# Kernel tuning notes

Measured on AMD Instinct MI355X. Metric: run time of the kernel, lower is better.

The kernel has to match this reference:

```python
import math
import jax, jax.numpy as jnp
import numpy as np

N_HEADS = 16
N_KV_HEADS = 4
HEAD_DIM = 64
DIM = 1024
WINDOW = 16
EPS = 0.01


def _alibi_slopes(n_heads):
    closest = 2 ** math.floor(math.log2(n_heads))
    base = 2.0 ** (-2.0 ** (-(math.log2(closest) - 3)))
    slopes = base ** np.arange(1, closest + 1, dtype=np.float32)
    if closest < n_heads:
        eb = 2.0 ** (-2.0 ** (-(math.log2(2 * closest) - 3)))
        extra = eb ** np.arange(1, 2 * (n_heads - closest) + 1, 2, dtype=np.float32)
        slopes = np.concatenate([slopes, extra])
    return jnp.asarray(slopes[:n_heads])


def _rmsnorm(x, w):
    xf = x.astype(jnp.float32)
    norm = jax.lax.rsqrt(jnp.mean(xf * xf, axis=-1, keepdims=True) + EPS)
    return (xf * norm).astype(x.dtype) * w


def setup_inputs() -> dict:
    key = jax.random.key(0)
    ks = jax.random.split(key, 6)
    B, L = 2, 2048
    s = 1.0 / math.sqrt(DIM)
    return {
        "x": jax.random.normal(ks[0], (B, L, DIM), jnp.float32),
        "wq": jax.random.normal(ks[1], (N_HEADS * HEAD_DIM, DIM), jnp.float32) * s,
        "wk": jax.random.normal(ks[2], (N_KV_HEADS * HEAD_DIM, DIM), jnp.float32) * s,
        "wv": jax.random.normal(ks[3], (N_KV_HEADS * HEAD_DIM, DIM), jnp.float32) * s,
        "wo": jax.random.normal(ks[4], (DIM, N_HEADS * HEAD_DIM), jnp.float32) * s,
        "q_norm_w": jnp.ones((HEAD_DIM,), jnp.float32),
        "k_norm_w": jnp.ones((HEAD_DIM,), jnp.float32),
    }


def reference(x, wq, wk, wv, wo, q_norm_w, k_norm_w):
    B, L, _ = x.shape
    n_rep = N_HEADS // N_KV_HEADS
    q = (x @ wq.T).reshape(B, L, N_HEADS, HEAD_DIM)
    k = (x @ wk.T).reshape(B, L, N_KV_HEADS, HEAD_DIM)
    v = (x @ wv.T).reshape(B, L, N_KV_HEADS, HEAD_DIM)
    q = _rmsnorm(q, q_norm_w)
    k = _rmsnorm(k, k_norm_w)
    # GQA repeat: head h maps to kv head (h % n_kv_heads), matching torch expand order
    k = jnp.broadcast_to(k[:, :, None], (B, L, n_rep, N_KV_HEADS, HEAD_DIM)).reshape(B, L, N_HEADS, HEAD_DIM)
    v = jnp.broadcast_to(v[:, :, None], (B, L, n_rep, N_KV_HEADS, HEAD_DIM)).reshape(B, L, N_HEADS, HEAD_DIM)
    # ALiBi bias with causal + sliding-window mask
    pos = jnp.arange(L)
    rel = pos[None, :] - pos[:, None]  # [L, L], j - i
    slopes = _alibi_slopes(N_HEADS)  # [H]
    bias = slopes[:, None, None] * rel[None].astype(jnp.float32)  # [H, L, L]
    masked = (rel > 0) | (rel < -WINDOW)
    bias = jnp.where(masked[None], -jnp.inf, bias)
    scale = 1.0 / math.sqrt(HEAD_DIM)
    attn = jnp.einsum("bqhd,bkhd->bhqk", q, k) * scale + bias[None]
    attn = jax.nn.softmax(attn, axis=-1)
    out = jnp.einsum("bhqk,bkhd->bqhd", attn, v).reshape(B, L, N_HEADS * HEAD_DIM)
    return out @ wo.T
```

## Files before the change

kernel.cpp:

```cpp
#include <hip/hip_runtime.h>
#include <math.h>

#define DIM 1024
#define NH 16
#define NKV 4
#define HD 64
#define WINDOW 16
#define EPS 0.01f

typedef __bf16 bf16_t;
typedef bf16_t bf16x8 __attribute__((ext_vector_type(8)));
typedef bf16_t bf16x4 __attribute__((ext_vector_type(4)));
typedef float f32x4 __attribute__((ext_vector_type(4)));

__global__ __launch_bounds__(256) void f2bf_all(const float* __restrict__ x,
                                                const float* __restrict__ wq,
                                                const float* __restrict__ wk,
                                                const float* __restrict__ wv,
                                                const float* __restrict__ wo,
                                                bf16_t* __restrict__ xb,
                                                bf16_t* __restrict__ wqkvb,
                                                bf16_t* __restrict__ wob) {
  int i = blockIdx.x * blockDim.x + threadIdx.x;
  const float* src;
  bf16_t* dst;
  int off;
  if (i < 1048576) { src = x; dst = xb; off = i; }
  else if (i < 1310720) { src = wq; dst = wqkvb; off = i - 1048576; }
  else if (i < 1376256) { src = wk; dst = wqkvb + (size_t)1024 * DIM; off = i - 1310720; }
  else if (i < 1441792) { src = wv; dst = wqkvb + (size_t)1280 * DIM; off = i - 1376256; }
  else { src = wo; dst = wob; off = i - 1441792; }
  float4 f = ((const float4*)src)[off];
  bf16x4 o = {(bf16_t)f.x, (bf16_t)f.y, (bf16_t)f.z, (bf16_t)f.w};
  ((bf16x4*)dst)[off] = o;
}


#define GEMM_STAGE(buf, Ag, Bg)                                                 \
  {                                                                             \
    _Pragma("unroll")                                                           \
    for (int it = 0; it < 4; it++) {                                            \
      int c = it * 256 + t;                                                     \
      int r = c >> 3;                                                           \
      int kc = ((c & 7) - r) & 7;                                               \
      __builtin_amdgcn_global_load_lds(                                         \
          (const __attribute__((address_space(1))) void*)((Ag) + (size_t)r * K + kc * 8), \
          (__attribute__((address_space(3))) void*)(As[buf] + c * 8), 16, 0, 0); \
    }                                                                           \
    _Pragma("unroll")                                                           \
    for (int it = 0; it < 2; it++) {                                            \
      int c = it * 256 + t;                                                     \
      int r = c >> 3;                                                           \
      int kc = ((c & 7) - r) & 7;                                               \
      __builtin_amdgcn_global_load_lds(                                         \
          (const __attribute__((address_space(1))) void*)((Bg) + (size_t)r * K + kc * 8), \
          (__attribute__((address_space(3))) void*)(Bs[buf] + c * 8), 16, 0, 0); \
    }                                                                           \
  }

#define GEMM_DBUF_LOOP(Aptr, Bptr)                                              \
  {                                                                             \
    const bf16_t* Abase = Aptr + (size_t)row0 * K;                              \
    const bf16_t* Bbase = Bptr + (size_t)col0 * K;                              \
    GEMM_STAGE(0, Abase, Bbase)                                                 \
    const int nIter = K >> 6;                                                   \
    for (int ki = 0; ki < nIter; ki++) {                                        \
      __syncthreads();                                                          \
      if (ki + 1 < nIter)                                                       \
        GEMM_STAGE((ki + 1) & 1, Abase + (ki + 1) * 64, Bbase + (ki + 1) * 64)  \
      const bf16_t* Ab = As[ki & 1];                                            \
      const bf16_t* Bb = Bs[ki & 1];                                            \
      _Pragma("unroll")                                                         \
      for (int h = 0; h < 2; h++) {                                             \
        bf16x8 af[2], bfr[4];                                                   \
        _Pragma("unroll")                                                       \
        for (int mi = 0; mi < 2; mi++) af[mi] = *(const bf16x8*)(Ab + aoff[h][mi]); \
        _Pragma("unroll")                                                       \
        for (int ni = 0; ni < 4; ni++) bfr[ni] = *(const bf16x8*)(Bb + boff[h][ni]); \
        _Pragma("unroll")                                                       \
        for (int mi = 0; mi < 2; mi++)                                          \
          _Pragma("unroll")                                                     \
          for (int ni = 0; ni < 4; ni++)                                        \
            acc[mi][ni] = __builtin_amdgcn_mfma_f32_16x16x32_bf16(af[mi], bfr[ni], \
                                                                  acc[mi][ni], 0, 0, 0); \
      }                                                                         \
    }                                                                           \
  }

#define GEMM_PROLOGUE(NBX, BYX)                                                 \
  const int t = threadIdx.x;                                                    \
  const int lane = t & 63;                                                      \
  const int wid = t >> 6;                                                       \
  const int xcd = blockIdx.x & 7;                                               \
  const int jj = blockIdx.x >> 3;                                               \
  const int bx = jj % (NBX);                                                    \
  const int row0 = (xcd * (BYX) + jj / (NBX)) * 128;                            \
  const int col0 = bx * 64;                                                     \
  const int wm = wid * 32;                                                      \
  const int lquad = lane >> 4;                                                  \
  const int lcol = lane & 15;                                                   \
  int aoff[2][2], boff[2][4];                                                   \
  _Pragma("unroll")                                                             \
  for (int h = 0; h < 2; h++) {                                                 \
    _Pragma("unroll")                                                           \
    for (int mi = 0; mi < 2; mi++) {                                            \
      int r = wm + mi * 16 + lcol;                                              \
      aoff[h][mi] = r * 64 + (((h * 4 + lquad) + r) & 7) * 8;                   \
    }                                                                           \
    _Pragma("unroll")                                                           \
    for (int ni = 0; ni < 4; ni++) {                                            \
      int r = ni * 16 + lcol;                                                   \
      boff[h][ni] = r * 64 + (((h * 4 + lquad) + r) & 7) * 8;                   \
    }                                                                           \
  }                                                                             \
  f32x4 acc[2][4] = {};

__global__ __launch_bounds__(256) void gemm_qkv_rms(const bf16_t* __restrict__ A,
                                                    const bf16_t* __restrict__ B,
                                                    bf16_t* __restrict__ C,
                                                    const float* __restrict__ qw,
                                                    const float* __restrict__ kw,
                                                    int M, int N, int K) {
  __shared__ bf16_t As[2][128 * 64];
  __shared__ bf16_t Bs[2][64 * 64];
  GEMM_PROLOGUE(24, 4)
  GEMM_DBUF_LOOP(A, B)

  const int hcol = bx;
  const bool isv = (hcol >= 20);
  float wreg[4];
  if (!isv) {
    const float* wp = (hcol < 16) ? qw : kw;
#pragma unroll
    for (int ni = 0; ni < 4; ni++) wreg[ni] = wp[ni * 16 + lcol];
  }

#pragma unroll
  for (int mi = 0; mi < 2; mi++) {
#pragma unroll
    for (int r = 0; r < 4; r++) {
      float norm = 1.0f;
      if (!isv) {
        float ss = 0.0f;
#pragma unroll
        for (int ni = 0; ni < 4; ni++) ss += acc[mi][ni][r] * acc[mi][ni][r];
#pragma unroll
        for (int off = 8; off >= 1; off >>= 1) ss += __shfl_xor(ss, off);
        norm = rsqrtf(ss * (1.0f / 64.0f) + EPS);
      }
      size_t base = (size_t)(row0 + wm + mi * 16 + lquad * 4 + r) * N + col0 + lcol;
#pragma unroll
      for (int ni = 0; ni < 4; ni++) {
        float v = acc[mi][ni][r] * norm;
        if (!isv) v *= wreg[ni];
        C[base + ni * 16] = (bf16_t)v;
      }
    }
  }
}

template <typename CT, int NBX, int BYX>
__global__ __launch_bounds__(256) void gemm_bf16(const bf16_t* __restrict__ A,
                                                 const bf16_t* __restrict__ B,
                                                 CT* __restrict__ C,
                                                 int M, int N, int K) {
  __shared__ bf16_t As[2][128 * 64];
  __shared__ bf16_t Bs[2][64 * 64];
  GEMM_PROLOGUE(NBX, BYX)
  GEMM_DBUF_LOOP(A, B)

#pragma unroll
  for (int mi = 0; mi < 2; mi++)
#pragma unroll
    for (int ni = 0; ni < 4; ni++) {
      size_t base = (size_t)(row0 + wm + mi * 16 + lquad * 4) * N + col0 + ni * 16 + lcol;
#pragma unroll
      for (int r = 0; r < 4; r++)
        C[base + (size_t)r * N] = (CT)acc[mi][ni][r];
    }
}

#define LKP 72
#define LVP 40

__global__ __launch_bounds__(1024) void attn_mfma(const bf16_t* __restrict__ qkv,
                                                  bf16_t* __restrict__ y) {
  __shared__ bf16_t Ks[4][32][LKP];
  __shared__ bf16_t VTs[4][64][LVP];
  __shared__ bf16_t Ps[16][16][LVP];

  const int t = threadIdx.x;
  const int lane = t & 63;
  const int w = t >> 6;
  const int b = blockIdx.x >> 7;
  const int i0loc = (blockIdx.x & 127) << 4;
  const int rowbase = b << 11;
  const int rowg0 = rowbase + i0loc;

  {
    int kvh = t >> 8;
    int key = (t >> 3) & 31;
    int dc = t & 7;
    int jloc = i0loc - 16 + key;
    int rg = rowbase + (jloc < 0 ? 0 : jloc);
    const bf16_t* src = qkv + (size_t)rg * 1536 + 1024 + kvh * 64 + dc * 8;
    bf16x8 kval = *(const bf16x8*)src;
    *(bf16x8*)(&Ks[kvh][key][dc * 8]) = kval;
    bf16x8 vval = *(const bf16x8*)(src + 256);
    int kslot = ((key >> 3) ^ (dc & 3)) * 8 + (key & 7);
#pragma unroll
    for (int e = 0; e < 8; e++) VTs[kvh][dc * 8 + e][kslot] = vval[e];
  }
  __syncthreads();

  const int col = lane & 15;
  const int quad = lane >> 4;
  const int h = w;
  const int kvh = w & 3;
  const float slope = exp2f(-0.5f * (float)(h + 1));

  bf16x8 kf[2][2];
#pragma unroll
  for (int kt = 0; kt < 2; kt++)
#pragma unroll
    for (int kc = 0; kc < 2; kc++)
      kf[kt][kc] = *(const bf16x8*)(&Ks[kvh][kt * 16 + col][kc * 32 + quad * 8]);
  bf16x8 vf[4];
#pragma unroll
  for (int nt = 0; nt < 4; nt++) {
    int dim = nt * 16 + col;
    int kchunk = quad ^ ((dim >> 3) & 3);
    vf[nt] = *(const bf16x8*)(&VTs[kvh][dim][kchunk * 8]);
  }

  const bf16_t* qrow = qkv + (size_t)(rowg0 + col) * 1536 + h * 64;
  bf16x8 qf0 = *(const bf16x8*)(qrow + quad * 8);
  bf16x8 qf1 = *(const bf16x8*)(qrow + 32 + quad * 8);

  f32x4 s0 = {}, s1 = {};
  s0 = __builtin_amdgcn_mfma_f32_16x16x32_bf16(qf0, kf[0][0], s0, 0, 0, 0);
  s0 = __builtin_amdgcn_mfma_f32_16x16x32_bf16(qf1, kf[0][1], s0, 0, 0, 0);
  s1 = __builtin_amdgcn_mfma_f32_16x16x32_bf16(qf0, kf[1][0], s1, 0, 0, 0);
  s1 = __builtin_amdgcn_mfma_f32_16x16x32_bf16(qf1, kf[1][1], s1, 0, 0, 0);

  const bool t0dead = (i0loc == 0);
  float sc0[4], sc1[4];
#pragma unroll
  for (int r = 0; r < 4; r++) {
    int rel0 = col - 16 - (quad * 4 + r);
    int rel1 = rel0 + 16;
    bool m0 = t0dead || (rel0 < -WINDOW);
    bool m1 = (rel1 > 0);
    sc0[r] = m0 ? -INFINITY : s0[r] * 0.125f + slope * (float)rel0;
    sc1[r] = m1 ? -INFINITY : s1[r] * 0.125f + slope * (float)rel1;
  }
  float mx[4], sum[4], p0[4], p1[4];
#pragma unroll
  for (int r = 0; r < 4; r++) mx[r] = fmaxf(sc0[r], sc1[r]);
#pragma unroll
  for (int off = 8; off >= 1; off >>= 1)
#pragma unroll
    for (int r = 0; r < 4; r++) mx[r] = fmaxf(mx[r], __shfl_xor(mx[r], off));
#pragma unroll
  for (int r = 0; r < 4; r++) {
    p0[r] = __expf(sc0[r] - mx[r]);
    p1[r] = __expf(sc1[r] - mx[r]);
    sum[r] = p0[r] + p1[r];
  }
#pragma unroll
  for (int off = 8; off >= 1; off >>= 1)
#pragma unroll
    for (int r = 0; r < 4; r++) sum[r] += __shfl_xor(sum[r], off);

#pragma unroll
  for (int r = 0; r < 4; r++) {
    Ps[w][quad * 4 + r][col] = (bf16_t)p0[r];
    Ps[w][quad * 4 + r][16 + col] = (bf16_t)p1[r];
  }
  bf16x8 pf = *(const bf16x8*)(&Ps[w][col][quad * 8]);

  f32x4 o[4] = {};
#pragma unroll
  for (int nt = 0; nt < 4; nt++)
    o[nt] = __builtin_amdgcn_mfma_f32_16x16x32_bf16(pf, vf[nt], o[nt], 0, 0, 0);

#pragma unroll
  for (int nt = 0; nt < 4; nt++)
#pragma unroll
    for (int r = 0; r < 4; r++)
      y[(size_t)(rowg0 + quad * 4 + r) * 1024 + h * 64 + nt * 16 + col] =
          (bf16_t)(o[nt][r] / sum[r]);
}

extern "C" void kernel_launch(void* const* d_in, const int* in_sizes, int n_in,
                              void* d_out, int out_size, void* d_ws, size_t ws_size,
                              hipStream_t stream) {
  const float* x  = (const float*)d_in[0];
  const float* wq = (const float*)d_in[1];
  const float* wk = (const float*)d_in[2];
  const float* wv = (const float*)d_in[3];
  const float* wo = (const float*)d_in[4];
  const float* qw = (const float*)d_in[5];
  const float* kw = (const float*)d_in[6];
  float* out = (float*)d_out;

  const int M = 4096;

  bf16_t* xb    = (bf16_t*)d_ws;
  bf16_t* wqkvb = xb + (size_t)M * DIM;
  bf16_t* wob   = wqkvb + (size_t)1536 * DIM;
  bf16_t* qkv   = wob + (size_t)DIM * DIM;
  bf16_t* yb    = qkv + (size_t)M * 1536;

  dim3 blk(256);
  f2bf_all<<<1703936 / 256, blk, 0, stream>>>(x, wq, wk, wv, wo, xb, wqkvb, wob);

  gemm_qkv_rms<<<768, blk, 0, stream>>>(xb, wqkvb, qkv, qw, kw, M, 1536, DIM);

  attn_mfma<<<256, dim3(1024), 0, stream>>>(qkv, yb);

  gemm_bf16<float, 16, 4><<<512, blk, 0, stream>>>(yb, wob, out, M, DIM, DIM);
}
```

Measured before the change: 126.8 us.

## Split GEMM K-halves across warp pairs with LDS reduction; hoist attention Q loads

Result: slower. 458.8 us (+261.7%).

```diff
diff --git a/kernel.cpp b/kernel.cpp
--- a/kernel.cpp
+++ b/kernel.cpp
@@ -70,21 +70,39 @@
         GEMM_STAGE((ki + 1) & 1, Abase + (ki + 1) * 64, Bbase + (ki + 1) * 64)  \
       const bf16_t* Ab = As[ki & 1];                                            \
       const bf16_t* Bb = Bs[ki & 1];                                            \
-      _Pragma("unroll")                                                         \
-      for (int h = 0; h < 2; h++) {                                             \
-        bf16x8 af[2], bfr[4];                                                   \
+      bf16x8 af[4], bfr[4];                                                     \
+      _Pragma("unroll")                                                         \
+      for (int mi = 0; mi < 4; mi++) af[mi] = *(const bf16x8*)(Ab + aoff[mi]);  \
+      _Pragma("unroll")                                                         \
+      for (int ni = 0; ni < 4; ni++) bfr[ni] = *(const bf16x8*)(Bb + boff[ni]); \
+      _Pragma("unroll")                                                         \
+      for (int mi = 0; mi < 4; mi++)                                            \
         _Pragma("unroll")                                                       \
-        for (int mi = 0; mi < 2; mi++) af[mi] = *(const bf16x8*)(Ab + aoff[h][mi]); \
-        _Pragma("unroll")                                                       \
-        for (int ni = 0; ni < 4; ni++) bfr[ni] = *(const bf16x8*)(Bb + boff[h][ni]); \
-        _Pragma("unroll")                                                       \
-        for (int mi = 0; mi < 2; mi++)                                          \
-          _Pragma("unroll")                                                     \
-          for (int ni = 0; ni < 4; ni++)                                        \
-            acc[mi][ni] = __builtin_amdgcn_mfma_f32_16x16x32_bf16(af[mi], bfr[ni], \
-                                                                  acc[mi][ni], 0, 0, 0); \
+        for (int ni = 0; ni < 4; ni++)                                          \
+          acc[mi][ni] = __builtin_amdgcn_mfma_f32_16x16x32_bf16(af[mi], bfr[ni], \
+                                                                acc[mi][ni], 0, 0, 0); \
+    }                                                                           \
+  }
+
+#define GEMM_REDUCE()                                                           \
+  {                                                                             \
+    float* Xs = (float*)smem;                                                   \
+    __syncthreads();                                                            \
+    _Pragma("unroll")                                                           \
+    for (int j = 0; j < 2; j++)                                                 \
+      _Pragma("unroll")                                                         \
+      for (int ni = 0; ni < 4; ni++)                                            \
+        *(f32x4*)(Xs + (size_t)(wid * 64 + ni * 16 + lcol) * 36 + j * 16 + lquad * 4) = \
+            acc[h0 ? j : 2 + j][ni];                                            \
+    __syncthreads();                                                            \
+    _Pragma("unroll")                                                           \
+    for (int j = 0; j < 2; j++)                                                 \
+      _Pragma("unroll")                                                         \
+      for (int ni = 0; ni < 4; ni++) {                                          \
+        f32x4 p = *(const f32x4*)(Xs + (size_t)((wid ^ 1) * 64 + ni * 16 + lcol) * 36 + \
+                                  j * 16 + lquad * 4);                          \
+        acc[j][ni] = (h0 ? acc[2 + j][ni] : acc[j][ni]) + p;                    \
       }                                                                         \
-    }                                                                           \
   }
 
 #define GEMM_PROLOGUE(NBX, BYX)                                                 \
@@ -96,35 +114,36 @@
   const int bx = jj % (NBX);                                                    \
   const int row0 = (xcd * (BYX) + jj / (NBX)) * 128;                            \
   const int col0 = bx * 64;                                                     \
+  const int pr = (wid >> 1) * 64;                                               \
+  const int h0 = wid & 1;                                                       \
   const int wm = wid * 32;                                                      \
   const int lquad = lane >> 4;                                                  \
   const int lcol = lane & 15;                                                   \
-  int aoff[2][2], boff[2][4];                                                   \
+  int aoff[4], boff[4];                                                         \
   _Pragma("unroll")                                                             \
-  for (int h = 0; h < 2; h++) {                                                 \
-    _Pragma("unroll")                                                           \
-    for (int mi = 0; mi < 2; mi++) {                                            \
-      int r = wm + mi * 16 + lcol;                                              \
-      aoff[h][mi] = r * 64 + (((h * 4 + lquad) + r) & 7) * 8;                   \
-    }                                                                           \
-    _Pragma("unroll")                                                           \
-    for (int ni = 0; ni < 4; ni++) {                                            \
-      int r = ni * 16 + lcol;                                                   \
-      boff[h][ni] = r * 64 + (((h * 4 + lquad) + r) & 7) * 8;                   \
-    }                                                                           \
+  for (int mi = 0; mi < 4; mi++) {                                              \
+    int r = pr + mi * 16 + lcol;                                                \
+    aoff[mi] = r * 64 + (((h0 * 4 + lquad) + r) & 7) * 8;                       \
   }                                                                             \
-  f32x4 acc[2][4] = {};
-
-__global__ __launch_bounds__(256) void gemm_qkv_rms(const bf16_t* __restrict__ A,
-                                                    const bf16_t* __restrict__ B,
-                                                    bf16_t* __restrict__ C,
-                                                    const float* __restrict__ qw,
-                                                    const float* __restrict__ kw,
-                                                    int M, int N, int K) {
-  __shared__ bf16_t As[2][128 * 64];
-  __shared__ bf16_t Bs[2][64 * 64];
+  _Pragma("unroll")                                                             \
+  for (int ni = 0; ni < 4; ni++) {                                              \
+    int r = ni * 16 + lcol;                                                     \
+    boff[ni] = r * 64 + (((h0 * 4 + lquad) + r) & 7) * 8;                       \
+  }                                                                             \
+  f32x4 acc[4][4] = {};
+
+__global__ __launch_bounds__(256, 3) void gemm_qkv_rms(const bf16_t* __restrict__ A,
+                                                       const bf16_t* __restrict__ B,
+                                                       bf16_t* __restrict__ C,
+                                                       const float* __restrict__ qw,
+                                                       const float* __restrict__ kw,
+                                                       int M, int N, int K) {
+  __shared__ __align__(16) char smem[49152];
+  bf16_t (*As)[128 * 64] = (bf16_t(*)[128 * 64])smem;
+  bf16_t (*Bs)[64 * 64] = (bf16_t(*)[64 * 64])(smem + 32768);
   GEMM_PROLOGUE(24, 4)
   GEMM_DBUF_LOOP(A, B)
+  GEMM_REDUCE()
 
   const int hcol = bx;
   const bool isv = (hcol >= 20);
@@ -160,14 +179,16 @@
 }
 
 template <typename CT, int NBX, int BYX>
-__global__ __launch_bounds__(256) void gemm_bf16(const bf16_t* __restrict__ A,
-                                                 const bf16_t* __restrict__ B,
-                                                 CT* __restrict__ C,
-                                                 int M, int N, int K) {
-  __shared__ bf16_t As[2][128 * 64];
-  __shared__ bf16_t Bs[2][64 * 64];
+__global__ __launch_bounds__(256, 3) void gemm_bf16(const bf16_t* __restrict__ A,
+                                                    const bf16_t* __restrict__ B,
+                                                    CT* __restrict__ C,
+                                                    int M, int N, int K) {
+  __shared__ __align__(16) char smem[49152];
+  bf16_t (*As)[128 * 64] = (bf16_t(*)[128 * 64])smem;
+  bf16_t (*Bs)[64 * 64] = (bf16_t(*)[64 * 64])(smem + 32768);
   GEMM_PROLOGUE(NBX, BYX)
   GEMM_DBUF_LOOP(A, B)
+  GEMM_REDUCE()
 
 #pragma unroll
   for (int mi = 0; mi < 2; mi++)
@@ -211,7 +232,6 @@
 #pragma unroll
     for (int e = 0; e < 8; e++) VTs[kvh][dc * 8 + e][kslot] = vval[e];
   }
-  __syncthreads();
 
   const int col = lane & 15;
   const int quad = lane >> 4;
@@ -219,6 +239,12 @@
   const int kvh = w & 3;
   const float slope = exp2f(-0.5f * (float)(h + 1));
 
+  const bf16_t* qrow = qkv + (size_t)(rowg0 + col) * 1536 + h * 64;
+  bf16x8 qf0 = *(const bf16x8*)(qrow + quad * 8);
+  bf16x8 qf1 = *(const bf16x8*)(qrow + 32 + quad * 8);
+
+  __syncthreads();
+
   bf16x8 kf[2][2];
 #pragma unroll
   for (int kt = 0; kt < 2; kt++)
@@ -232,10 +258,6 @@
     int kchunk = quad ^ ((dim >> 3) & 3);
     vf[nt] = *(const bf16x8*)(&VTs[kvh][dim][kchunk * 8]);
   }
-
-  const bf16_t* qrow = qkv + (size_t)(rowg0 + col) * 1536 + h * 64;
-  bf16x8 qf0 = *(const bf16x8*)(qrow + quad * 8);
-  bf16x8 qf1 = *(const bf16x8*)(qrow + 32 + quad * 8);
 
   f32x4 s0 = {}, s1 = {};
   s0 = __builtin_amdgcn_mfma_f32_16x16x32_bf16(qf0, kf[0][0], s0, 0, 0, 0);
```
